# Optimization experiments

Hardware: AMD Instinct MI355X
Metric: run time of the kernel (lower is better)

## Reference

```python
import jax, jax.numpy as jnp
import numpy as np

B, N, M, C, S = 4, 16384, 128, 128, 512  # batch, points, boxes, feat dim, sampled pts


def setup_inputs() -> dict:
    key = jax.random.key(0)
    k1, k2, k3, k4, k5, k6, k7 = jax.random.split(key, 7)
    # point cloud roughly in a LiDAR extent
    xy = jax.random.uniform(k1, (B, N, 2), minval=-50.0, maxval=50.0)
    z = jax.random.uniform(k2, (B, N, 1), minval=-3.0, maxval=3.0)
    points = jnp.concatenate([xy, z], axis=-1).astype(jnp.float32)
    point_features = jax.random.normal(k3, (B, N, C), dtype=jnp.float32)
    # boxes: (cx, cy, cz_bottom, dx, dy, dz, rz)
    ctr_xy = jax.random.uniform(k4, (B, M, 2), minval=-50.0, maxval=50.0)
    ctr_z = jax.random.uniform(k5, (B, M, 1), minval=-3.0, maxval=0.0)
    sizes = jax.random.uniform(k6, (B, M, 3), minval=2.0, maxval=8.0)
    rz = jax.random.uniform(k7, (B, M, 1), minval=-np.pi, maxval=np.pi)
    boxes3d = jnp.concatenate([ctr_xy, ctr_z, sizes, rz], axis=-1).astype(jnp.float32)
    return {"points": points, "point_features": point_features, "boxes3d": boxes3d}


def _pool_one_box(points, feats, box):
    # points (N,3), feats (N,C), box (7,)
    n = points.shape[0]
    cx, cy, cz, dx, dy, dz, rz = box
    cz = cz + 0.5 * dz  # bottom center -> geometric center (mmcv convention)
    sx = points[:, 0] - cx
    sy = points[:, 1] - cy
    cosa = jnp.cos(-rz)
    sina = jnp.sin(-rz)
    lx = sx * cosa - sy * sina
    ly = sx * sina + sy * cosa
    mask = (
        (jnp.abs(points[:, 2] - cz) <= 0.5 * dz)
        & (lx > -0.5 * dx) & (lx < 0.5 * dx)
        & (ly > -0.5 * dy) & (ly < 0.5 * dy)
    )
    cnt = mask.sum(dtype=jnp.int32)
    # rank of each in-box point among in-box points (first-come order)
    rank = jnp.cumsum(mask.astype(jnp.int32)) - 1
    pos = jnp.where(mask, rank, n)  # out-of-range for non-members -> dropped
    table = jnp.zeros((n,), jnp.int32).at[pos].set(
        jnp.arange(n, dtype=jnp.int32), mode="drop")
    # wrap-around duplication when cnt < S (kernel copies k % cnt)
    j = jnp.arange(S, dtype=jnp.int32) % jnp.maximum(cnt, 1)
    idx = table[j]  # (S,)
    pooled = jnp.concatenate([points[idx], feats[idx]], axis=-1)  # (S, 3+C)
    pooled = jnp.where(cnt > 0, pooled, jnp.zeros_like(pooled))
    empty = (cnt == 0).astype(jnp.int32)
    return pooled, empty


def reference(points, point_features, boxes3d):
    # vmap over boxes, then over batch
    per_scene = jax.vmap(_pool_one_box, in_axes=(None, None, 0))
    per_batch = jax.vmap(per_scene, in_axes=(0, 0, 0))
    pooled_features, pooled_empty_flag = per_batch(points, point_features, boxes3d)
    return pooled_features, pooled_empty_flag
```

## Files before the change

### kernel.cpp

```cpp
#include <hip/hip_runtime.h>

#define B_ 4
#define N_ 16384
#define M_ 128
#define C_ 128
#define S_ 512
#define ROW_ 131
#define NCHUNK_ 256
#define TILE_ 128
#define LSTR_ 136
#define KBOX_ 4

typedef float f4_t __attribute__((ext_vector_type(4)));

__device__ __forceinline__ int swz(int j, int col) {
    return j * LSTR_ + (col & 3) * 34 + (col >> 2);
}

__global__ __launch_bounds__(256) void mask_kernel(
    const float* __restrict__ points,
    const float* __restrict__ boxes,
    unsigned long long* __restrict__ masks)
{
    const int gwave = blockIdx.x * 4 + (threadIdx.x >> 6);
    const int lane  = threadIdx.x & 63;
    const int grp   = gwave >> 4;
    const int seg   = gwave & 15;
    const int bm0   = grp * KBOX_;
    const int b     = bm0 >> 7;

    const float* pb = points + (size_t)b * N_ * 3;
    float px[16], py[16], pz[16];
    #pragma unroll
    for (int k = 0; k < 16; ++k) {
        const int i = (seg * 16 + k) * 64 + lane;
        px[k] = pb[i*3+0]; py[k] = pb[i*3+1]; pz[k] = pb[i*3+2];
    }

    for (int kb = 0; kb < KBOX_; ++kb) {
        const int bm = bm0 + kb;
        const float* bx = boxes + bm * 7;
        const float cx = bx[0], cy = bx[1], czb = bx[2];
        const float dx = bx[3], dy = bx[4], dzv = bx[5], rz = bx[6];
        const float cz   = __fadd_rn(czb, __fmul_rn(0.5f, dzv));
        const float cosa = (float)cos(-(double)rz);
        const float sina = (float)sin(-(double)rz);
        const float hdx = 0.5f * dx, hdy = 0.5f * dy, hdz = 0.5f * dzv;

        #pragma unroll
        for (int k = 0; k < 16; ++k) {
            const float sx = __fsub_rn(px[k], cx);
            const float sy = __fsub_rn(py[k], cy);
            const float lx = __fsub_rn(__fmul_rn(sx, cosa), __fmul_rn(sy, sina));
            const float ly = __fadd_rn(__fmul_rn(sx, sina), __fmul_rn(sy, cosa));
            const bool pred = (fabsf(__fsub_rn(pz[k], cz)) <= hdz) &&
                              (lx > -hdx) && (lx < hdx) &&
                              (ly > -hdy) && (ly < hdy);
            const unsigned long long m = __ballot(pred);
            if (lane == 0) masks[(size_t)bm * NCHUNK_ + seg * 16 + k] = m;
        }
    }
}

__global__ __launch_bounds__(512, 4) void pool_kernel(
    const float* __restrict__ points,
    const float* __restrict__ feats,
    const unsigned long long* __restrict__ masks,
    float* __restrict__ out,
    float* __restrict__ flags_out)
{
    const int bm   = blockIdx.x;
    const int b    = bm >> 7;
    const int tid  = threadIdx.x;
    const int w    = tid >> 6;
    const int lane = tid & 63;

    __shared__ int   s_wsum[4];
    __shared__ int   s_idx[S_];
    __shared__ int   jtab[S_ + 1];
    __shared__ float srow[TILE_ * LSTR_];

    unsigned long long m0 = 0;
    int c = 0, Ppart = 0;
    if (tid < 256) {
        m0 = masks[(size_t)bm * NCHUNK_ + tid];
        c  = __popcll(m0);
        int incl = c;
        #pragma unroll
        for (int d = 1; d < 64; d <<= 1) {
            const int t = __shfl_up(incl, d, 64);
            if (lane >= d) incl += t;
        }
        if (lane == 63) s_wsum[w] = incl;
        Ppart = incl - c;
    }
    __syncthreads();
    const int w0 = s_wsum[0], w1 = s_wsum[1], w2 = s_wsum[2], w3 = s_wsum[3];
    const int total = w0 + w1 + w2 + w3;

    if (tid < 256 && c > 0) {
        const int woff = (w > 0 ? w0 : 0) + (w > 1 ? w1 : 0) + (w > 2 ? w2 : 0);
        int pos = Ppart + woff;
        if (pos < S_) {
            unsigned long long m = m0;
            while (m && pos < S_) {
                const int bit = __ffsll((unsigned long long)m) - 1;
                m &= m - 1;
                s_idx[pos++] = tid * 64 + bit;
            }
        }
    }

    const int cnt_eff = total < S_ ? total : S_;
    const int denom   = cnt_eff > 0 ? cnt_eff : 1;
    for (int s = tid; s <= S_; s += 512)
        jtab[s] = (s < S_) ? (int)((unsigned)s % (unsigned)denom) : 0;
    __syncthreads();

    const int T = cnt_eff < TILE_ ? cnt_eff : TILE_;
    if (total == 0) {
        if (tid < LSTR_) srow[tid] = 0.0f;
    } else {
        const int nf4 = T * 32;
        for (int t = tid; t < nf4; t += 512) {
            const int u = t >> 5, q = t & 31;
            const size_t pbase = (size_t)b * N_ + (unsigned)s_idx[u];
            const f4_t v = *(const f4_t*)(feats + pbase * C_ + q * 4);
            #pragma unroll
            for (int jj = 0; jj < 4; ++jj)
                srow[swz(u, 3 + 4 * q + jj)] = v[jj];
        }
        for (int t = tid; t < T * 3; t += 512) {
            const int u = t / 3, k = t - u * 3;
            const size_t pbase = (size_t)b * N_ + (unsigned)s_idx[u];
            srow[swz(u, k)] = points[pbase * 3 + k];
        }
    }
    __syncthreads();

    float* ob = out + (size_t)bm * (S_ * ROW_);
    if (cnt_eff <= TILE_) {
        #pragma unroll 1
        for (int bt = 0; bt < 4; ++bt) {
            f4_t v[8];
            #pragma unroll
            for (int u = 0; u < 8; ++u) {
                const int e = 4 * (tid + (bt * 8 + u) * 512);
                const unsigned s0 = (unsigned)e / (unsigned)ROW_;
                const int col0 = e - (int)s0 * ROW_;
                const int ja = jtab[s0], jb = jtab[s0 + 1];
                #pragma unroll
                for (int jj = 0; jj < 4; ++jj) {
                    int col = col0 + jj;
                    const bool cross = col >= ROW_;
                    col = cross ? col - ROW_ : col;
                    const int j = cross ? jb : ja;
                    v[u][jj] = srow[swz(j, col)];
                }
            }
            #pragma unroll
            for (int u = 0; u < 8; ++u) {
                const int e = 4 * (tid + (bt * 8 + u) * 512);
                *(f4_t*)(ob + e) = v[u];
            }
        }
        if (tid < 384) {
            const int e = 4 * (tid + 16384);
            const unsigned s0 = (unsigned)e / (unsigned)ROW_;
            const int col0 = e - (int)s0 * ROW_;
            const int ja = jtab[s0], jb = jtab[s0 + 1];
            f4_t v;
            #pragma unroll
            for (int jj = 0; jj < 4; ++jj) {
                int col = col0 + jj;
                const bool cross = col >= ROW_;
                col = cross ? col - ROW_ : col;
                const int j = cross ? jb : ja;
                v[jj] = srow[swz(j, col)];
            }
            *(f4_t*)(ob + e) = v;
        }
    } else {
        for (int f = tid; f < (S_ * ROW_) / 4; f += 512) {
            const int e = 4 * f;
            const unsigned s0 = (unsigned)e / (unsigned)ROW_;
            const int col0 = e - (int)s0 * ROW_;
            f4_t v;
            #pragma unroll
            for (int jj = 0; jj < 4; ++jj) {
                int col = col0 + jj;
                unsigned s = s0;
                if (col >= ROW_) { col -= ROW_; ++s; }
                const int j = jtab[s];
                float val;
                if (j < TILE_) {
                    val = srow[swz(j, col)];
                } else {
                    const size_t pbase = (size_t)b * N_ + (unsigned)s_idx[j];
                    val = (col < 3) ? points[pbase * 3 + col]
                                    : feats[pbase * C_ + (col - 3)];
                }
                v[jj] = val;
            }
            *(f4_t*)(ob + e) = v;
        }
    }
    if (tid == 0) flags_out[bm] = (total == 0) ? 1.0f : 0.0f;
}

extern "C" void kernel_launch(void* const* d_in, const int* in_sizes, int n_in,
                              void* d_out, int out_size, void* d_ws, size_t ws_size,
                              hipStream_t stream) {
    const float* points = (const float*)d_in[0];
    const float* feats  = (const float*)d_in[1];
    const float* boxes  = (const float*)d_in[2];
    float* out = (float*)d_out;

    unsigned long long* masks = (unsigned long long*)d_ws;

    float* flags = out + (size_t)B_ * M_ * S_ * ROW_;

    mask_kernel<<<B_ * M_ * 16 / 4 / KBOX_, 256, 0, stream>>>(
        points, boxes, masks);
    pool_kernel<<<B_ * M_, 512, 0, stream>>>(points, feats, masks, out, flags);
}
```

Measured before the change: 171.6 us.

## Fuse mask and pool kernels with inter-block flag synchronization

Merges the mask-computation kernel and the pooling kernel into a single 512-block launch of 256 threads. Each block computes a quarter of the masks for a group of four boxes, publishes them through an atomic ready flag, and spins until the other three blocks in its group finish before pooling its own box. This removes a kernel launch and the gap between launches, but adds a memset launch, spin-waiting that assumes co-residency of all four blocks, and halves the threads per block for the pooling phase.

```diff
diff --git a/kernel.cpp b/kernel.cpp
--- a/kernel.cpp
+++ b/kernel.cpp
@@ -17,103 +17,108 @@
     return j * LSTR_ + (col & 3) * 34 + (col >> 2);
 }
 
-__global__ __launch_bounds__(256) void mask_kernel(
-    const float* __restrict__ points,
-    const float* __restrict__ boxes,
-    unsigned long long* __restrict__ masks)
-{
-    const int gwave = blockIdx.x * 4 + (threadIdx.x >> 6);
-    const int lane  = threadIdx.x & 63;
-    const int grp   = gwave >> 4;
-    const int seg   = gwave & 15;
-    const int bm0   = grp * KBOX_;
-    const int b     = bm0 >> 7;
-
-    const float* pb = points + (size_t)b * N_ * 3;
-    float px[16], py[16], pz[16];
-    #pragma unroll
-    for (int k = 0; k < 16; ++k) {
-        const int i = (seg * 16 + k) * 64 + lane;
-        px[k] = pb[i*3+0]; py[k] = pb[i*3+1]; pz[k] = pb[i*3+2];
-    }
-
-    for (int kb = 0; kb < KBOX_; ++kb) {
-        const int bm = bm0 + kb;
-        const float* bx = boxes + bm * 7;
-        const float cx = bx[0], cy = bx[1], czb = bx[2];
-        const float dx = bx[3], dy = bx[4], dzv = bx[5], rz = bx[6];
-        const float cz   = __fadd_rn(czb, __fmul_rn(0.5f, dzv));
-        const float cosa = (float)cos(-(double)rz);
-        const float sina = (float)sin(-(double)rz);
-        const float hdx = 0.5f * dx, hdy = 0.5f * dy, hdz = 0.5f * dzv;
-
-        #pragma unroll
-        for (int k = 0; k < 16; ++k) {
-            const float sx = __fsub_rn(px[k], cx);
-            const float sy = __fsub_rn(py[k], cy);
-            const float lx = __fsub_rn(__fmul_rn(sx, cosa), __fmul_rn(sy, sina));
-            const float ly = __fadd_rn(__fmul_rn(sx, sina), __fmul_rn(sy, cosa));
-            const bool pred = (fabsf(__fsub_rn(pz[k], cz)) <= hdz) &&
-                              (lx > -hdx) && (lx < hdx) &&
-                              (ly > -hdy) && (ly < hdy);
-            const unsigned long long m = __ballot(pred);
-            if (lane == 0) masks[(size_t)bm * NCHUNK_ + seg * 16 + k] = m;
-        }
-    }
-}
-
-__global__ __launch_bounds__(512, 4) void pool_kernel(
+__global__ __launch_bounds__(256) void fused_kernel(
     const float* __restrict__ points,
     const float* __restrict__ feats,
-    const unsigned long long* __restrict__ masks,
+    const float* __restrict__ boxes,
+    unsigned long long* __restrict__ masks,
+    int* __restrict__ ready,
     float* __restrict__ out,
     float* __restrict__ flags_out)
 {
-    const int bm   = blockIdx.x;
-    const int b    = bm >> 7;
+    const int g    = blockIdx.x;
     const int tid  = threadIdx.x;
     const int w    = tid >> 6;
     const int lane = tid & 63;
+    const int k    = g >> 2;
 
     __shared__ int   s_wsum[4];
     __shared__ int   s_idx[S_];
     __shared__ int   jtab[S_ + 1];
     __shared__ float srow[TILE_ * LSTR_];
 
-    unsigned long long m0 = 0;
-    int c = 0, Ppart = 0;
-    if (tid < 256) {
-        m0 = masks[(size_t)bm * NCHUNK_ + tid];
-        c  = __popcll(m0);
-        int incl = c;
+    {
+        const int gwave = g * 4 + w;
+        const int grp   = gwave >> 4;
+        const int seg   = gwave & 15;
+        const int bm0   = grp * KBOX_;
+        const int b     = bm0 >> 7;
+
+        const float* pb = points + (size_t)b * N_ * 3;
+        float px[16], py[16], pz[16];
         #pragma unroll
-        for (int d = 1; d < 64; d <<= 1) {
-            const int t = __shfl_up(incl, d, 64);
-            if (lane >= d) incl += t;
-        }
-        if (lane == 63) s_wsum[w] = incl;
-        Ppart = incl - c;
-    }
+        for (int kk = 0; kk < 16; ++kk) {
+            const int i = (seg * 16 + kk) * 64 + lane;
+            px[kk] = pb[i*3+0]; py[kk] = pb[i*3+1]; pz[kk] = pb[i*3+2];
+        }
+
+        for (int kb = 0; kb < KBOX_; ++kb) {
+            const int bm = bm0 + kb;
+            const float* bx = boxes + bm * 7;
+            const float cx = bx[0], cy = bx[1], czb = bx[2];
+            const float dx = bx[3], dy = bx[4], dzv = bx[5], rz = bx[6];
+            const float cz   = __fadd_rn(czb, __fmul_rn(0.5f, dzv));
+            const float cosa = (float)cos(-(double)rz);
+            const float sina = (float)sin(-(double)rz);
+            const float hdx = 0.5f * dx, hdy = 0.5f * dy, hdz = 0.5f * dzv;
+
+            #pragma unroll
+            for (int kk = 0; kk < 16; ++kk) {
+                const float sx = __fsub_rn(px[kk], cx);
+                const float sy = __fsub_rn(py[kk], cy);
+                const float lx = __fsub_rn(__fmul_rn(sx, cosa), __fmul_rn(sy, sina));
+                const float ly = __fadd_rn(__fmul_rn(sx, sina), __fmul_rn(sy, cosa));
+                const bool pred = (fabsf(__fsub_rn(pz[kk], cz)) <= hdz) &&
+                                  (lx > -hdx) && (lx < hdx) &&
+                                  (ly > -hdy) && (ly < hdy);
+                const unsigned long long m = __ballot(pred);
+                if (lane == 0) masks[(size_t)bm * NCHUNK_ + seg * 16 + kk] = m;
+            }
+        }
+    }
+
+    __syncthreads();
+    if (tid == 0) {
+        __threadfence();
+        atomicOr(&ready[k], 1 << (g & 3));
+        while ((__hip_atomic_load(&ready[k], __ATOMIC_ACQUIRE,
+                                  __HIP_MEMORY_SCOPE_AGENT) & 15) != 15)
+            __builtin_amdgcn_s_sleep(8);
+    }
+    __syncthreads();
+    __threadfence();
+
+    const int bm = g;
+    const int b  = bm >> 7;
+
+    const unsigned long long m0 = masks[(size_t)bm * NCHUNK_ + tid];
+    const int c = __popcll(m0);
+
+    int incl = c;
+    #pragma unroll
+    for (int d = 1; d < 64; d <<= 1) {
+        const int t = __shfl_up(incl, d, 64);
+        if (lane >= d) incl += t;
+    }
+    if (lane == 63) s_wsum[w] = incl;
     __syncthreads();
     const int w0 = s_wsum[0], w1 = s_wsum[1], w2 = s_wsum[2], w3 = s_wsum[3];
+    const int woff  = (w > 0 ? w0 : 0) + (w > 1 ? w1 : 0) + (w > 2 ? w2 : 0);
     const int total = w0 + w1 + w2 + w3;
-
-    if (tid < 256 && c > 0) {
-        const int woff = (w > 0 ? w0 : 0) + (w > 1 ? w1 : 0) + (w > 2 ? w2 : 0);
-        int pos = Ppart + woff;
-        if (pos < S_) {
-            unsigned long long m = m0;
-            while (m && pos < S_) {
-                const int bit = __ffsll((unsigned long long)m) - 1;
-                m &= m - 1;
-                s_idx[pos++] = tid * 64 + bit;
-            }
+    int pos = incl - c + woff;
+
+    if (c > 0 && pos < S_) {
+        unsigned long long m = m0;
+        while (m && pos < S_) {
+            const int bit = __ffsll((unsigned long long)m) - 1;
+            m &= m - 1;
+            s_idx[pos++] = tid * 64 + bit;
         }
     }
 
     const int cnt_eff = total < S_ ? total : S_;
     const int denom   = cnt_eff > 0 ? cnt_eff : 1;
-    for (int s = tid; s <= S_; s += 512)
+    for (int s = tid; s <= S_; s += 256)
         jtab[s] = (s < S_) ? (int)((unsigned)s % (unsigned)denom) : 0;
     __syncthreads();
 
@@ -122,7 +127,7 @@
         if (tid < LSTR_) srow[tid] = 0.0f;
     } else {
         const int nf4 = T * 32;
-        for (int t = tid; t < nf4; t += 512) {
+        for (int t = tid; t < nf4; t += 256) {
             const int u = t >> 5, q = t & 31;
             const size_t pbase = (size_t)b * N_ + (unsigned)s_idx[u];
             const f4_t v = *(const f4_t*)(feats + pbase * C_ + q * 4);
@@ -130,10 +135,10 @@
             for (int jj = 0; jj < 4; ++jj)
                 srow[swz(u, 3 + 4 * q + jj)] = v[jj];
         }
-        for (int t = tid; t < T * 3; t += 512) {
-            const int u = t / 3, k = t - u * 3;
+        for (int t = tid; t < T * 3; t += 256) {
+            const int u = t / 3, kk = t - u * 3;
             const size_t pbase = (size_t)b * N_ + (unsigned)s_idx[u];
-            srow[swz(u, k)] = points[pbase * 3 + k];
+            srow[swz(u, kk)] = points[pbase * 3 + kk];
         }
     }
     __syncthreads();
@@ -141,11 +146,11 @@
     float* ob = out + (size_t)bm * (S_ * ROW_);
     if (cnt_eff <= TILE_) {
         #pragma unroll 1
-        for (int bt = 0; bt < 4; ++bt) {
+        for (int bt = 0; bt < 8; ++bt) {
             f4_t v[8];
             #pragma unroll
             for (int u = 0; u < 8; ++u) {
-                const int e = 4 * (tid + (bt * 8 + u) * 512);
+                const int e = 4 * (tid + (bt * 8 + u) * 256);
                 const unsigned s0 = (unsigned)e / (unsigned)ROW_;
                 const int col0 = e - (int)s0 * ROW_;
                 const int ja = jtab[s0], jb = jtab[s0 + 1];
@@ -160,12 +165,12 @@
             }
             #pragma unroll
             for (int u = 0; u < 8; ++u) {
-                const int e = 4 * (tid + (bt * 8 + u) * 512);
+                const int e = 4 * (tid + (bt * 8 + u) * 256);
                 *(f4_t*)(ob + e) = v[u];
             }
         }
-        if (tid < 384) {
-            const int e = 4 * (tid + 16384);
+        for (int f = 16384 + tid; f < 16768; f += 256) {
+            const int e = 4 * f;
             const unsigned s0 = (unsigned)e / (unsigned)ROW_;
             const int col0 = e - (int)s0 * ROW_;
             const int ja = jtab[s0], jb = jtab[s0 + 1];
@@ -181,7 +186,7 @@
             *(f4_t*)(ob + e) = v;
         }
     } else {
-        for (int f = tid; f < (S_ * ROW_) / 4; f += 512) {
+        for (int f = tid; f < (S_ * ROW_) / 4; f += 256) {
             const int e = 4 * f;
             const unsigned s0 = (unsigned)e / (unsigned)ROW_;
             const int col0 = e - (int)s0 * ROW_;
@@ -216,11 +221,13 @@
     const float* boxes  = (const float*)d_in[2];
     float* out = (float*)d_out;
 
-    unsigned long long* masks = (unsigned long long*)d_ws;
+    char* ws = (char*)d_ws;
+    unsigned long long* masks = (unsigned long long*)ws;
+    int* ready = (int*)(ws + (size_t)B_ * M_ * NCHUNK_ * 8);
 
     float* flags = out + (size_t)B_ * M_ * S_ * ROW_;
 
-    mask_kernel<<<B_ * M_ * 16 / 4 / KBOX_, 256, 0, stream>>>(
-        points, boxes, masks);
-    pool_kernel<<<B_ * M_, 512, 0, stream>>>(points, feats, masks, out, flags);
+    hipMemsetAsync(ready, 0, (B_ * M_ / KBOX_) * sizeof(int), stream);
+    fused_kernel<<<B_ * M_, 256, 0, stream>>>(
+        points, feats, boxes, masks, ready, out, flags);
 }
```

Result: slower. 230.3 us (+34.2%).

## Fuse point-in-box mask computation into pool kernel via LDS masks

Applied to the files above, without the earlier changes.

Removes the separate mask kernel and computes each box's membership ballots inside the pooling block, storing the 256 mask words in shared memory instead of a global workspace. This drops one kernel launch and the global write and readback of the masks. In exchange, each block now reads all 16384 points of its scene (mostly served from L2), and the mask phase runs serially before pooling within each block.

```diff
diff --git a/kernel.cpp b/kernel.cpp
--- a/kernel.cpp
+++ b/kernel.cpp
@@ -9,7 +9,6 @@
 #define NCHUNK_ 256
 #define TILE_ 128
 #define LSTR_ 136
-#define KBOX_ 4
 
 typedef float f4_t __attribute__((ext_vector_type(4)));
 
@@ -17,55 +16,10 @@
     return j * LSTR_ + (col & 3) * 34 + (col >> 2);
 }
 
-__global__ __launch_bounds__(256) void mask_kernel(
-    const float* __restrict__ points,
-    const float* __restrict__ boxes,
-    unsigned long long* __restrict__ masks)
-{
-    const int gwave = blockIdx.x * 4 + (threadIdx.x >> 6);
-    const int lane  = threadIdx.x & 63;
-    const int grp   = gwave >> 4;
-    const int seg   = gwave & 15;
-    const int bm0   = grp * KBOX_;
-    const int b     = bm0 >> 7;
-
-    const float* pb = points + (size_t)b * N_ * 3;
-    float px[16], py[16], pz[16];
-    #pragma unroll
-    for (int k = 0; k < 16; ++k) {
-        const int i = (seg * 16 + k) * 64 + lane;
-        px[k] = pb[i*3+0]; py[k] = pb[i*3+1]; pz[k] = pb[i*3+2];
-    }
-
-    for (int kb = 0; kb < KBOX_; ++kb) {
-        const int bm = bm0 + kb;
-        const float* bx = boxes + bm * 7;
-        const float cx = bx[0], cy = bx[1], czb = bx[2];
-        const float dx = bx[3], dy = bx[4], dzv = bx[5], rz = bx[6];
-        const float cz   = __fadd_rn(czb, __fmul_rn(0.5f, dzv));
-        const float cosa = (float)cos(-(double)rz);
-        const float sina = (float)sin(-(double)rz);
-        const float hdx = 0.5f * dx, hdy = 0.5f * dy, hdz = 0.5f * dzv;
-
-        #pragma unroll
-        for (int k = 0; k < 16; ++k) {
-            const float sx = __fsub_rn(px[k], cx);
-            const float sy = __fsub_rn(py[k], cy);
-            const float lx = __fsub_rn(__fmul_rn(sx, cosa), __fmul_rn(sy, sina));
-            const float ly = __fadd_rn(__fmul_rn(sx, sina), __fmul_rn(sy, cosa));
-            const bool pred = (fabsf(__fsub_rn(pz[k], cz)) <= hdz) &&
-                              (lx > -hdx) && (lx < hdx) &&
-                              (ly > -hdy) && (ly < hdy);
-            const unsigned long long m = __ballot(pred);
-            if (lane == 0) masks[(size_t)bm * NCHUNK_ + seg * 16 + k] = m;
-        }
-    }
-}
-
-__global__ __launch_bounds__(512, 4) void pool_kernel(
+__global__ __launch_bounds__(512, 4) void fused_kernel(
     const float* __restrict__ points,
     const float* __restrict__ feats,
-    const unsigned long long* __restrict__ masks,
+    const float* __restrict__ boxes,
     float* __restrict__ out,
     float* __restrict__ flags_out)
 {
@@ -75,15 +29,42 @@
     const int w    = tid >> 6;
     const int lane = tid & 63;
 
+    __shared__ unsigned long long mlds[NCHUNK_];
     __shared__ int   s_wsum[4];
     __shared__ int   s_idx[S_];
     __shared__ int   jtab[S_ + 1];
     __shared__ float srow[TILE_ * LSTR_];
 
+    const float* bx = boxes + bm * 7;
+    const float cx = bx[0], cy = bx[1], czb = bx[2];
+    const float dx = bx[3], dy = bx[4], dzv = bx[5], rz = bx[6];
+    const float cz   = __fadd_rn(czb, __fmul_rn(0.5f, dzv));
+    const float cosa = (float)cos(-(double)rz);
+    const float sina = (float)sin(-(double)rz);
+    const float hdx = 0.5f * dx, hdy = 0.5f * dy, hdz = 0.5f * dzv;
+
+    const float* pb = points + (size_t)b * N_ * 3;
+    #pragma unroll 4
+    for (int cc = 0; cc < 32; ++cc) {
+        const int ch = w * 32 + cc;
+        const int i  = ch * 64 + lane;
+        const float x = pb[i*3+0], y = pb[i*3+1], z = pb[i*3+2];
+        const float sx = __fsub_rn(x, cx);
+        const float sy = __fsub_rn(y, cy);
+        const float lx = __fsub_rn(__fmul_rn(sx, cosa), __fmul_rn(sy, sina));
+        const float ly = __fadd_rn(__fmul_rn(sx, sina), __fmul_rn(sy, cosa));
+        const bool pred = (fabsf(__fsub_rn(z, cz)) <= hdz) &&
+                          (lx > -hdx) && (lx < hdx) &&
+                          (ly > -hdy) && (ly < hdy);
+        const unsigned long long m = __ballot(pred);
+        if (lane == 0) mlds[ch] = m;
+    }
+    __syncthreads();
+
     unsigned long long m0 = 0;
     int c = 0, Ppart = 0;
     if (tid < 256) {
-        m0 = masks[(size_t)bm * NCHUNK_ + tid];
+        m0 = mlds[tid];
         c  = __popcll(m0);
         int incl = c;
         #pragma unroll
@@ -216,11 +197,8 @@
     const float* boxes  = (const float*)d_in[2];
     float* out = (float*)d_out;
 
-    unsigned long long* masks = (unsigned long long*)d_ws;
-
     float* flags = out + (size_t)B_ * M_ * S_ * ROW_;
 
-    mask_kernel<<<B_ * M_ * 16 / 4 / KBOX_, 256, 0, stream>>>(
-        points, boxes, masks);
-    pool_kernel<<<B_ * M_, 512, 0, stream>>>(points, feats, masks, out, flags);
+    fused_kernel<<<B_ * M_, 512, 0, stream>>>(
+        points, feats, boxes, out, flags);
 }
```

Measured after the change: 176.8 us. 1.03x slower.
